# Optimization experiments

Measured on AMD Instinct MI355X. Metric: run time of the kernel, lower is better.

## Reference

```python
import jax, jax.numpy as jnp
import numpy as np

BLOCK_SIZE = 32
# E2M1 (FP4) representable magnitudes and rounding midpoints
FP4_GRID = jnp.array([0.0, 0.5, 1.0, 1.5, 2.0, 3.0, 4.0, 6.0], dtype=jnp.float32)
FP4_MIDS = jnp.array([0.25, 0.75, 1.25, 1.75, 2.5, 3.5, 5.0], dtype=jnp.float32)


def quantize_to_mxfp4(w, block_size=BLOCK_SIZE):
    """Quantize (K, N) weight to MXFP4: per-block-of-32 (along K) power-of-2 scale
    + E2M1 codes. Returns dequantized-code tensor q (K//bs, bs, N) and scales
    (K//bs, 1, N) so that dequant = q * scales."""
    K, N = w.shape
    wb = w.reshape(K // block_size, block_size, N)
    amax = jnp.max(jnp.abs(wb), axis=1, keepdims=True)          # (K//bs, 1, N)
    # E8M0 scale: 2^(floor(log2(amax)) - 2) so amax/scale falls in [4, 8) -> clipped to 6
    exp = jnp.floor(jnp.log2(jnp.maximum(amax, 1e-30))) - 2.0
    scales = jnp.exp2(exp)
    x = wb / scales
    idx = jnp.digitize(jnp.abs(x), FP4_MIDS)                    # round-to-nearest FP4 magnitude
    q = jnp.sign(x) * FP4_GRID[idx]
    return q, scales


def mxfp4_matmul(inputs, q, scales, block_size=BLOCK_SIZE):
    """inputs: (..., K); q: (K//bs, bs, N); scales: (K//bs, 1, N)."""
    K = inputs.shape[-1]
    N = q.shape[-1]
    w = (q * scales).reshape(K, N)   # fused dequant (reference form)
    return inputs @ w


def setup_inputs() -> dict:
    key = jax.random.key(0)
    ks = jax.random.split(key, 3)
    B, S, D, F = 4, 2048, 2048, 8192
    inputs = jax.random.normal(ks[0], (B, S, D), dtype=jnp.float32)
    up_kernel = jax.random.normal(ks[1], (D, F), dtype=jnp.float32) * (1.0 / np.sqrt(D))
    down_kernel = jax.random.normal(ks[2], (F, D), dtype=jnp.float32) * (1.0 / np.sqrt(F))
    up_bias = jnp.zeros((F,), dtype=jnp.float32)
    down_bias = jnp.zeros((D,), dtype=jnp.float32)
    return {"inputs": inputs, "up_kernel": up_kernel, "up_bias": up_bias,
            "down_kernel": down_kernel, "down_bias": down_bias}


def reference(inputs, up_kernel, up_bias, down_kernel, down_bias):
    q_up, s_up = quantize_to_mxfp4(up_kernel, BLOCK_SIZE)
    x = mxfp4_matmul(inputs, q_up, s_up, BLOCK_SIZE) + up_bias
    x = jax.nn.gelu(x)
    q_dn, s_dn = quantize_to_mxfp4(down_kernel, BLOCK_SIZE)
    x = mxfp4_matmul(x, q_dn, s_dn, BLOCK_SIZE) + down_bias
    return x
```

## Files before the change

kernel.cpp:

```cpp
#include <hip/hip_runtime.h>
#include <hip/hip_bf16.h>

typedef __bf16 bf16_t;
typedef __attribute__((ext_vector_type(8))) __bf16 bf16x8;
typedef __attribute__((ext_vector_type(4))) float f32x4;
typedef __attribute__((ext_vector_type(4))) unsigned int u32x4;

__device__ __forceinline__ void gload_lds16(const bf16_t* g, bf16_t* l) {
    __builtin_amdgcn_global_load_lds(
        (const __attribute__((address_space(1))) void*)g,
        (__attribute__((address_space(3))) void*)l,
        16, 0, 0);
}

__device__ __forceinline__ float gelu_f(float v) {
    float u = 0.7978845608028654f * (v + 0.044715f * v * v * v);
    float e = __expf(-2.f * u);
    float t = __fdividef(1.f - e, 1.f + e);
    return 0.5f * v * (1.f + t);
}

__device__ __forceinline__ void quant_one(const float* __restrict__ w,
                                          bf16_t* __restrict__ wt,
                                          int K, int N, int tix) {
    int n = tix % N;
    int b = tix / N;
    const float* src = w + (size_t)b * 32 * N + n;
    float v[32];
    float amax = 0.f;
#pragma unroll
    for (int i = 0; i < 32; ++i) {
        v[i] = __builtin_nontemporal_load(src + (size_t)i * N);
        amax = fmaxf(amax, fabsf(v[i]));
    }
    unsigned eb = (__float_as_uint(amax) >> 23) & 0xFF;
    float scale = __uint_as_float((eb - 2u) << 23);
    float inv   = __uint_as_float((256u - eb) << 23);
    if (amax == 0.f) { scale = 0.f; inv = 0.f; }
    bf16_t dq[32];
#pragma unroll
    for (int i = 0; i < 32; ++i) {
        float x  = v[i] * inv;
        float ax = fabsf(x);
        float q = ax < 0.25f ? 0.0f : ax < 0.75f ? 0.5f : ax < 1.25f ? 1.0f :
                  ax < 1.75f ? 1.5f : ax < 2.5f  ? 2.0f : ax < 3.5f  ? 3.0f :
                  ax < 5.0f  ? 4.0f : 6.0f;
        float d = copysignf(q * scale, x);
        dq[i] = (bf16_t)d;
    }
    const int r  = n & 255, rt = n >> 8, kt = b >> 1, ub = (b & 1) * 4;
    bf16_t* base = wt + (((size_t)rt * (K >> 6) + kt) << 14) + (r << 6);
#pragma unroll
    for (int j = 0; j < 4; ++j) {
        bf16x8 p;
#pragma unroll
        for (int t = 0; t < 8; ++t) p[t] = dq[j * 8 + t];
        *(bf16x8*)(base + (((ub + j) ^ (r & 7)) << 3)) = p;
    }
}

__global__ void prep_kernel(const float* __restrict__ in, bf16_t* __restrict__ out,
                            int ncvt, int cvtB, int dLog,
                            const float* __restrict__ upw, bf16_t* __restrict__ upwt,
                            int upK, int upN, int qupB,
                            const float* __restrict__ dnw, bf16_t* __restrict__ dnwt,
                            int dnK, int dnN) {
    int bid = blockIdx.x;
    if (bid < cvtB) {
        int i = (bid * blockDim.x + threadIdx.x) << 3;
        if (i >= ncvt) return;
        const f32x4* p = (const f32x4*)(in + i);
        f32x4 a = __builtin_nontemporal_load(p);
        f32x4 b = __builtin_nontemporal_load(p + 1);
        bf16x8 o;
        o[0] = (bf16_t)a[0]; o[1] = (bf16_t)a[1]; o[2] = (bf16_t)a[2]; o[3] = (bf16_t)a[3];
        o[4] = (bf16_t)b[0]; o[5] = (bf16_t)b[1]; o[6] = (bf16_t)b[2]; o[7] = (bf16_t)b[3];
        const int row = i >> dLog, d = i & ((1 << dLog) - 1);
        const int r = row & 255, mt = row >> 8, dt = d >> 6, u = (d >> 3) & 7;
        size_t off = (((size_t)mt * (1 << (dLog - 6)) + dt) << 14) + (r << 6)
                     + ((u ^ (r & 7)) << 3);
        *(bf16x8*)(out + off) = o;
    } else if (bid < cvtB + qupB) {
        int tix = (bid - cvtB) * blockDim.x + threadIdx.x;
        if (tix >= (upK >> 5) * upN) return;
        quant_one(upw, upwt, upK, upN, tix);
    } else {
        int tix = (bid - cvtB - qupB) * blockDim.x + threadIdx.x;
        if (tix >= (dnK >> 5) * dnN) return;
        quant_one(dnw, dnwt, dnK, dnN, tix);
    }
}

#define VMW4  asm volatile("s_waitcnt vmcnt(4)" ::: "memory")
#define VMW0  asm volatile("s_waitcnt vmcnt(0)" ::: "memory")
#define BARR  asm volatile("s_barrier" ::: "memory")
#define LGKM0 asm volatile("s_waitcnt lgkmcnt(0)" ::: "memory")

#define MFMA_ROW(MI, A0, A1)                                                          \
    acc[MI][0] = __builtin_amdgcn_mfma_f32_16x16x32_bf16(A0, bf00, acc[MI][0],0,0,0); \
    acc[MI][0] = __builtin_amdgcn_mfma_f32_16x16x32_bf16(A1, bf01, acc[MI][0],0,0,0); \
    acc[MI][1] = __builtin_amdgcn_mfma_f32_16x16x32_bf16(A0, bf10, acc[MI][1],0,0,0); \
    acc[MI][1] = __builtin_amdgcn_mfma_f32_16x16x32_bf16(A1, bf11, acc[MI][1],0,0,0); \
    acc[MI][2] = __builtin_amdgcn_mfma_f32_16x16x32_bf16(A0, bf20, acc[MI][2],0,0,0); \
    acc[MI][2] = __builtin_amdgcn_mfma_f32_16x16x32_bf16(A1, bf21, acc[MI][2],0,0,0); \
    acc[MI][3] = __builtin_amdgcn_mfma_f32_16x16x32_bf16(A0, bf30, acc[MI][3],0,0,0); \
    acc[MI][3] = __builtin_amdgcn_mfma_f32_16x16x32_bf16(A1, bf31, acc[MI][3],0,0,0);

#define PHASE(BUF, P, STAGE_STMT, TAIL_STMT)                                          \
  {                                                                                   \
    af00 = lda(BUF, 2*(P),   0); af01 = lda(BUF, 2*(P),   1);                         \
    af10 = lda(BUF, 2*(P)+1, 0); af11 = lda(BUF, 2*(P)+1, 1);                         \
    if ((P) == 0) {                                                                   \
      bf00 = ldb(BUF,0,0); bf01 = ldb(BUF,0,1);                                       \
      bf10 = ldb(BUF,1,0); bf11 = ldb(BUF,1,1);                                       \
      bf20 = ldb(BUF,2,0); bf21 = ldb(BUF,2,1);                                       \
      bf30 = ldb(BUF,3,0); bf31 = ldb(BUF,3,1);                                       \
    }                                                                                 \
    STAGE_STMT;                                                                       \
    BARR;                                                                             \
    LGKM0;                                                                            \
    __builtin_amdgcn_s_setprio(1);                                                    \
    MFMA_ROW(2*(P),   af00, af01);                                                    \
    MFMA_ROW(2*(P)+1, af10, af11);                                                    \
    __builtin_amdgcn_s_setprio(0);                                                    \
    TAIL_STMT;                                                                        \
    BARR;                                                                             \
  }

template <int EPI, int MAP>
__global__ __launch_bounds__(512, 2)
void gemm_kernel(const bf16_t* __restrict__ A, const bf16_t* __restrict__ Bt,
                 const float* __restrict__ bias, void* __restrict__ Cout,
                 int M, int N, int K) {
    __shared__ __align__(16) char smem[131072];
    bf16_t* sAp = (bf16_t*)smem;
    bf16_t* sBp = (bf16_t*)(smem + 65536);
    const int tid     = threadIdx.x;
    const int lane    = tid & 63;
    const int wv      = tid >> 6;
    const int wr      = wv >> 2;
    const int wc      = wv & 3;
    const int laneLow = lane & 15;
    const int laneHi  = lane >> 4;

    int bm, bn;
    const int bid = blockIdx.x;
    if (MAP == 1) {
        const int xcd = bid & 7;
        const int l   = bid >> 3;
        const int r   = l >> 5;
        const int u   = l & 31;
        bm = r * 8 + ((xcd >> 2) << 2) + (u >> 3);
        bn = ((xcd & 3) << 3) + (u & 7);
    } else {
        const int ntn = N >> 8;
        const int nwg = gridDim.x;
        int wg  = (bid & 7) * (nwg >> 3) + (bid >> 3);
        bm = wg / ntn; bn = wg % ntn;
    }

    const int kT = K >> 6;

    auto stageA = [&](int b, int kt, int h) {
        const bf16_t* s = A + (((size_t)bm * kT + kt) << 14)
                            + ((h * 128 + wv * 8) << 6) + lane * 8;
        gload_lds16(s,        &sAp[b * 16384 + (h * 128 + wv * 8) * 64]);
        gload_lds16(s + 4096, &sAp[b * 16384 + (h * 128 + 64 + wv * 8) * 64]);
    };
    auto stageB = [&](int b, int kt, int h) {
        const bf16_t* s = Bt + (((size_t)bn * kT + kt) << 14)
                             + ((h * 128 + wv * 8) << 6) + lane * 8;
        gload_lds16(s,        &sBp[b * 16384 + (h * 128 + wv * 8) * 64]);
        gload_lds16(s + 4096, &sBp[b * 16384 + (h * 128 + 64 + wv * 8) * 64]);
    };

    const int s7  = laneLow & 7;
    const int xk0 = ((laneHi) ^ s7) << 3;
    const int xk1 = ((4 + laneHi) ^ s7) << 3;
    const int aOffBase = (wr * 128 + laneLow) * 64;
    const int bOffBase = (wc * 64 + laneLow) * 64;
    auto lda = [&](int b, int m, int ks) -> bf16x8 {
        return *(const bf16x8*)(&sAp[b * 16384 + aOffBase + m * 1024 + (ks ? xk1 : xk0)]);
    };
    auto ldb = [&](int b, int n2, int ks) -> bf16x8 {
        return *(const bf16x8*)(&sBp[b * 16384 + bOffBase + n2 * 1024 + (ks ? xk1 : xk0)]);
    };

    f32x4 acc[8][4];
#pragma unroll
    for (int i = 0; i < 8; ++i)
#pragma unroll
        for (int j = 0; j < 4; ++j) acc[i][j] = (f32x4){0.f, 0.f, 0.f, 0.f};

    bf16x8 af00, af01, af10, af11;
    bf16x8 bf00, bf01, bf10, bf11, bf20, bf21, bf30, bf31;

    stageA(0, 0, 0); stageA(0, 0, 1);
    stageB(0, 0, 0); stageB(0, 0, 1);
    stageB(1, 1, 0); stageB(1, 1, 1);
    VMW4;
    BARR;

    const int niter = kT >> 1;
    for (int i = 0; i < niter; ++i) {
        const bool nlast = (i + 1 < niter);
        const int kO  = 2 * i + 1;
        const int kN  = 2 * i + 2;
        const int kN1 = 2 * i + 3;
        PHASE(0, 0, stageA(1, kO, 0), ((void)0));
        PHASE(0, 1, stageA(1, kO, 1), ((void)0));
        PHASE(0, 2, if (nlast) stageB(0, kN, 0), ((void)0));
        PHASE(0, 3, if (nlast) stageB(0, kN, 1),
              if (nlast) { VMW4; } else { VMW0; });
        PHASE(1, 0, if (nlast) stageA(0, kN, 0), ((void)0));
        PHASE(1, 1, if (nlast) stageA(0, kN, 1), ((void)0));
        PHASE(1, 2, if (nlast) stageB(1, kN1, 0), ((void)0));
        PHASE(1, 3, if (nlast) stageB(1, kN1, 1),
              if (nlast) { VMW4; });
    }

    if (EPI == 0) {
        char* sC = smem;
#pragma unroll
        for (int n = 0; n < 4; ++n) {
            const int colL = wc * 64 + n * 16 + laneLow;
            const float bv = bias[bn * 256 + colL];
            const int u6   = (colL >> 3) & 7;
#pragma unroll
            for (int m = 0; m < 8; ++m) {
#pragma unroll
                for (int j = 0; j < 4; ++j) {
                    const int rowL = wr * 128 + m * 16 + (laneHi << 2) + j;
                    float v = acc[m][n][j] + bv;
                    int byte = ((colL >> 6) << 15) + (rowL << 7)
                             + ((u6 ^ (rowL & 7)) << 4) + ((colL & 7) << 1);
                    byte ^= ((rowL >> 2) & 3) << 5;
                    *(bf16_t*)(sC + byte) = (bf16_t)gelu_f(v);
                }
            }
        }
        LGKM0;
        BARR;
        char* dst = (char*)Cout + (((size_t)bm * (N >> 6) + bn * 4) << 15);
#pragma unroll
        for (int s = 0; s < 16; ++s) {
            int lin = s * 8192 + tid * 16;
            int row = (lin >> 7) & 255;
            int rb  = lin ^ (((row >> 2) & 3) << 5);
            u32x4 v = *(const u32x4*)(sC + rb);
            __builtin_nontemporal_store(v, (u32x4*)(dst + lin));
        }
    } else {
        const int r0 = bm * 256 + wr * 128 + (laneHi << 2);
        const int c0 = bn * 256 + wc * 64 + laneLow;
        float* Cf = (float*)Cout;
#pragma unroll
        for (int n = 0; n < 4; ++n) {
            const int col = c0 + n * 16;
            const float bv = bias[col];
#pragma unroll
            for (int m = 0; m < 8; ++m) {
#pragma unroll
                for (int j = 0; j < 4; ++j) {
                    const int row = r0 + m * 16 + j;
                    __builtin_nontemporal_store(acc[m][n][j] + bv,
                                                &Cf[(size_t)row * N + col]);
                }
            }
        }
    }
}

extern "C" void kernel_launch(void* const* d_in, const int* in_sizes, int n_in,
                              void* d_out, int out_size, void* d_ws, size_t ws_size,
                              hipStream_t stream) {
    const float* inputs = (const float*)d_in[0];
    const float* up_w   = (const float*)d_in[1];
    const float* up_b   = (const float*)d_in[2];
    const float* dn_w   = (const float*)d_in[3];
    const float* dn_b   = (const float*)d_in[4];
    float* out = (float*)d_out;

    const int D = in_sizes[4];
    const int F = in_sizes[2];
    const int M = in_sizes[0] / D;
    const int dLog = 31 - __builtin_clz((unsigned)D);

    size_t r0_bytes = (size_t)(M > F ? M : F) * D * 2;
    char* ws = (char*)d_ws;
    bf16_t* in_bf = (bf16_t*)ws;
    bf16_t* wup_t = (bf16_t*)(ws + r0_bytes);
    bf16_t* mid   = (bf16_t*)(ws + r0_bytes + (size_t)F * D * 2);
    bf16_t* wdn_t = (bf16_t*)(ws + r0_bytes + (size_t)F * D * 2 + (size_t)M * F * 2);

    int ncvt = M * D;
    int cvtB = ncvt / (8 * 256);
    int qupB = ((D / 32) * F + 255) / 256;
    int qdnB = ((F / 32) * D + 255) / 256;
    prep_kernel<<<cvtB + qupB + qdnB, 256, 0, stream>>>(
        inputs, in_bf, ncvt, cvtB, dLog,
        up_w, wup_t, D, F, qupB,
        dn_w, wdn_t, F, D);

    gemm_kernel<0, 1><<<(M / 256) * (F / 256), 512, 0, stream>>>(
        in_bf, wup_t, up_b, (void*)mid, M, F, D);

    gemm_kernel<1, 0><<<(M / 256) * (D / 256), 512, 0, stream>>>(
        mid, wdn_t, dn_b, (void*)out, M, D, F);
    (void)ws_size; (void)n_in; (void)out_size;
}
```

Measured before the change: 536.4 us.

## Use 256x128 single-buffered tile kernel for the up-projection GEMM

Replaces the templated 256x256 eight-phase pipelined GEMM for the first matmul with a dedicated kernel. The new kernel uses 256x128 tiles, 64 KB of LDS and 4 waves per SIMD in its launch bounds, so more blocks can be resident per CU, and it uses a new XCD-aware block mapping. Each k-tile is loaded, fully waited on, then computed, so there is no software prefetch overlapping loads with MFMA work. The aim is to rely on occupancy to hide memory latency, at the cost of losing explicit pipelining and getting less operand reuse per tile. The down-projection kernel is de-templated and otherwise left unchanged.

```diff
diff --git a/kernel.cpp b/kernel.cpp
--- a/kernel.cpp
+++ b/kernel.cpp
@@ -96,6 +96,116 @@
 #define BARR  asm volatile("s_barrier" ::: "memory")
 #define LGKM0 asm volatile("s_waitcnt lgkmcnt(0)" ::: "memory")
 
+__global__ __launch_bounds__(512, 4)
+void gemm1_kernel(const bf16_t* __restrict__ A, const bf16_t* __restrict__ Bt,
+                  const float* __restrict__ bias, bf16_t* __restrict__ C,
+                  int M, int N, int K) {
+    __shared__ __align__(16) char smem[65536];
+    bf16_t* sAp = (bf16_t*)smem;
+    bf16_t* sBp = (bf16_t*)(smem + 32768);
+    const int tid     = threadIdx.x;
+    const int lane    = tid & 63;
+    const int wv      = tid >> 6;
+    const int wr      = wv >> 1;
+    const int wc      = wv & 1;
+    const int laneLow = lane & 15;
+    const int laneHi  = lane >> 4;
+
+    const int bid = blockIdx.x;
+    const int xcd = bid & 7, l = bid >> 3, r = l >> 5, u = l & 31;
+    const int bm = ((xcd & 1) << 3) + (u >> 2) + ((r & 1) << 4);
+    const int bn = ((xcd >> 1) << 2) + (u & 3) + ((r >> 1) << 4);
+
+    const int kT = K >> 6;
+    const int rtB = bn >> 1;
+    const size_t bHalf = (size_t)(bn & 1) << 13;
+
+    auto stageA = [&](int kt) {
+        const bf16_t* s = A + (((size_t)bm * kT + kt) << 14)
+                            + ((wv * 8) << 6) + lane * 8;
+#pragma unroll
+        for (int h = 0; h < 2; ++h) {
+            gload_lds16(s + h * 8192,        &sAp[(h * 128 + wv * 8) * 64]);
+            gload_lds16(s + h * 8192 + 4096, &sAp[(h * 128 + 64 + wv * 8) * 64]);
+        }
+    };
+    auto stageB = [&](int kt) {
+        const bf16_t* s = Bt + (((size_t)rtB * kT + kt) << 14) + bHalf
+                             + ((wv * 8) << 6) + lane * 8;
+        gload_lds16(s,        &sBp[(wv * 8) * 64]);
+        gload_lds16(s + 4096, &sBp[(64 + wv * 8) * 64]);
+    };
+
+    const int s7  = laneLow & 7;
+    const int xk0 = ((laneHi) ^ s7) << 3;
+    const int xk1 = ((4 + laneHi) ^ s7) << 3;
+    const int aOffBase = (wr * 64 + laneLow) * 64;
+    const int bOffBase = (wc * 64 + laneLow) * 64;
+
+    f32x4 acc[4][4];
+#pragma unroll
+    for (int i = 0; i < 4; ++i)
+#pragma unroll
+        for (int j = 0; j < 4; ++j) acc[i][j] = (f32x4){0.f, 0.f, 0.f, 0.f};
+
+#pragma unroll 1
+    for (int kt = 0; kt < kT; ++kt) {
+        stageA(kt); stageB(kt);
+        VMW0;
+        BARR;
+        __builtin_amdgcn_s_setprio(1);
+#pragma unroll
+        for (int ks = 0; ks < 2; ++ks) {
+            const int xk = ks ? xk1 : xk0;
+            bf16x8 b0 = *(const bf16x8*)(&sBp[bOffBase + 0 * 1024 + xk]);
+            bf16x8 b1 = *(const bf16x8*)(&sBp[bOffBase + 1 * 1024 + xk]);
+            bf16x8 b2 = *(const bf16x8*)(&sBp[bOffBase + 2 * 1024 + xk]);
+            bf16x8 b3 = *(const bf16x8*)(&sBp[bOffBase + 3 * 1024 + xk]);
+#pragma unroll
+            for (int m = 0; m < 4; ++m) {
+                bf16x8 a = *(const bf16x8*)(&sAp[aOffBase + m * 1024 + xk]);
+                acc[m][0] = __builtin_amdgcn_mfma_f32_16x16x32_bf16(a, b0, acc[m][0], 0, 0, 0);
+                acc[m][1] = __builtin_amdgcn_mfma_f32_16x16x32_bf16(a, b1, acc[m][1], 0, 0, 0);
+                acc[m][2] = __builtin_amdgcn_mfma_f32_16x16x32_bf16(a, b2, acc[m][2], 0, 0, 0);
+                acc[m][3] = __builtin_amdgcn_mfma_f32_16x16x32_bf16(a, b3, acc[m][3], 0, 0, 0);
+            }
+        }
+        __builtin_amdgcn_s_setprio(0);
+        BARR;
+    }
+
+    char* sC = smem;
+#pragma unroll
+    for (int n = 0; n < 4; ++n) {
+        const int colL = wc * 64 + n * 16 + laneLow;
+        const float bv = bias[bn * 128 + colL];
+        const int u6   = (colL >> 3) & 7;
+#pragma unroll
+        for (int m = 0; m < 4; ++m) {
+#pragma unroll
+            for (int j = 0; j < 4; ++j) {
+                const int rowL = wr * 64 + m * 16 + (laneHi << 2) + j;
+                float v = acc[m][n][j] + bv;
+                int byte = ((colL >> 6) << 15) + (rowL << 7)
+                         + ((u6 ^ (rowL & 7)) << 4) + ((colL & 7) << 1);
+                byte ^= ((rowL >> 2) & 3) << 5;
+                *(bf16_t*)(sC + byte) = (bf16_t)gelu_f(v);
+            }
+        }
+    }
+    LGKM0;
+    BARR;
+    char* dst = (char*)C + (((size_t)bm * (N >> 6) + bn * 2) << 15);
+#pragma unroll
+    for (int s = 0; s < 8; ++s) {
+        int lin = s * 8192 + tid * 16;
+        int row = (lin >> 7) & 255;
+        int rb  = lin ^ (((row >> 2) & 3) << 5);
+        u32x4 v = *(const u32x4*)(sC + rb);
+        __builtin_nontemporal_store(v, (u32x4*)(dst + lin));
+    }
+}
+
 #define MFMA_ROW(MI, A0, A1)                                                          \
     acc[MI][0] = __builtin_amdgcn_mfma_f32_16x16x32_bf16(A0, bf00, acc[MI][0],0,0,0); \
     acc[MI][0] = __builtin_amdgcn_mfma_f32_16x16x32_bf16(A1, bf01, acc[MI][0],0,0,0); \
@@ -127,11 +237,10 @@
     BARR;                                                                             \
   }
 
-template <int EPI, int MAP>
 __global__ __launch_bounds__(512, 2)
-void gemm_kernel(const bf16_t* __restrict__ A, const bf16_t* __restrict__ Bt,
-                 const float* __restrict__ bias, void* __restrict__ Cout,
-                 int M, int N, int K) {
+void gemm2_kernel(const bf16_t* __restrict__ A, const bf16_t* __restrict__ Bt,
+                  const float* __restrict__ bias, float* __restrict__ Cf,
+                  int M, int N, int K) {
     __shared__ __align__(16) char smem[131072];
     bf16_t* sAp = (bf16_t*)smem;
     bf16_t* sBp = (bf16_t*)(smem + 65536);
@@ -143,21 +252,11 @@
     const int laneLow = lane & 15;
     const int laneHi  = lane >> 4;
 
-    int bm, bn;
+    const int ntn = N >> 8;
+    const int nwg = gridDim.x;
     const int bid = blockIdx.x;
-    if (MAP == 1) {
-        const int xcd = bid & 7;
-        const int l   = bid >> 3;
-        const int r   = l >> 5;
-        const int u   = l & 31;
-        bm = r * 8 + ((xcd >> 2) << 2) + (u >> 3);
-        bn = ((xcd & 3) << 3) + (u & 7);
-    } else {
-        const int ntn = N >> 8;
-        const int nwg = gridDim.x;
-        int wg  = (bid & 7) * (nwg >> 3) + (bid >> 3);
-        bm = wg / ntn; bn = wg % ntn;
-    }
+    int wg  = (bid & 7) * (nwg >> 3) + (bid >> 3);
+    const int bm = wg / ntn, bn = wg % ntn;
 
     const int kT = K >> 6;
 
@@ -219,53 +318,19 @@
               if (nlast) { VMW4; });
     }
 
-    if (EPI == 0) {
-        char* sC = smem;
-#pragma unroll
-        for (int n = 0; n < 4; ++n) {
-            const int colL = wc * 64 + n * 16 + laneLow;
-            const float bv = bias[bn * 256 + colL];
-            const int u6   = (colL >> 3) & 7;
-#pragma unroll
-            for (int m = 0; m < 8; ++m) {
-#pragma unroll
-                for (int j = 0; j < 4; ++j) {
-                    const int rowL = wr * 128 + m * 16 + (laneHi << 2) + j;
-                    float v = acc[m][n][j] + bv;
-                    int byte = ((colL >> 6) << 15) + (rowL << 7)
-                             + ((u6 ^ (rowL & 7)) << 4) + ((colL & 7) << 1);
-                    byte ^= ((rowL >> 2) & 3) << 5;
-                    *(bf16_t*)(sC + byte) = (bf16_t)gelu_f(v);
-                }
-            }
-        }
-        LGKM0;
-        BARR;
-        char* dst = (char*)Cout + (((size_t)bm * (N >> 6) + bn * 4) << 15);
-#pragma unroll
-        for (int s = 0; s < 16; ++s) {
-            int lin = s * 8192 + tid * 16;
-            int row = (lin >> 7) & 255;
-            int rb  = lin ^ (((row >> 2) & 3) << 5);
-            u32x4 v = *(const u32x4*)(sC + rb);
-            __builtin_nontemporal_store(v, (u32x4*)(dst + lin));
-        }
-    } else {
-        const int r0 = bm * 256 + wr * 128 + (laneHi << 2);
-        const int c0 = bn * 256 + wc * 64 + laneLow;
-        float* Cf = (float*)Cout;
-#pragma unroll
-        for (int n = 0; n < 4; ++n) {
-            const int col = c0 + n * 16;
-            const float bv = bias[col];
-#pragma unroll
-            for (int m = 0; m < 8; ++m) {
-#pragma unroll
-                for (int j = 0; j < 4; ++j) {
-                    const int row = r0 + m * 16 + j;
-                    __builtin_nontemporal_store(acc[m][n][j] + bv,
-                                                &Cf[(size_t)row * N + col]);
-                }
+    const int r0 = bm * 256 + wr * 128 + (laneHi << 2);
+    const int c0 = bn * 256 + wc * 64 + laneLow;
+#pragma unroll
+    for (int n = 0; n < 4; ++n) {
+        const int col = c0 + n * 16;
+        const float bv = bias[col];
+#pragma unroll
+        for (int m = 0; m < 8; ++m) {
+#pragma unroll
+            for (int j = 0; j < 4; ++j) {
+                const int row = r0 + m * 16 + j;
+                __builtin_nontemporal_store(acc[m][n][j] + bv,
+                                            &Cf[(size_t)row * N + col]);
             }
         }
     }
@@ -302,10 +367,10 @@
         up_w, wup_t, D, F, qupB,
         dn_w, wdn_t, F, D);
 
-    gemm_kernel<0, 1><<<(M / 256) * (F / 256), 512, 0, stream>>>(
-        in_bf, wup_t, up_b, (void*)mid, M, F, D);
-
-    gemm_kernel<1, 0><<<(M / 256) * (D / 256), 512, 0, stream>>>(
-        mid, wdn_t, dn_b, (void*)out, M, D, F);
+    gemm1_kernel<<<(M / 256) * (F / 128), 512, 0, stream>>>(
+        in_bf, wup_t, up_b, mid, M, F, D);
+
+    gemm2_kernel<<<(M / 256) * (D / 256), 512, 0, stream>>>(
+        mid, wdn_t, dn_b, out, M, D, F);
     (void)ws_size; (void)n_in; (void)out_size;
 }
```

New measurement: 531.6 us, median of 2. Within noise of the previous version (-0.9%).
